# Kernel tuning notes

Hardware: AMD Instinct MI355X
Metric: run time of the kernel (lower is better)

The kernel has to match this reference:

```python
import jax, jax.numpy as jnp
import numpy as np

H, HKV, D = 32, 8, 128          # query heads, kv heads, head dim
G = H // HKV                     # GQA group size
PAGE, TOPK = 64, 64              # page size, top-k pages per (b, kv-head)
SCALE = D ** -0.5


def rotate_half(x):
    x1, x2 = x[..., : x.shape[-1] // 2], x[..., x.shape[-1] // 2 :]
    return jnp.concatenate((-x2, x1), axis=-1)


def setup_inputs() -> dict:
    key = jax.random.key(0)
    ks = jax.random.split(key, 8)
    B, Q, HID, S = 4, 1, 4096, 16384
    hidden_states = jax.random.normal(ks[0], (B, Q, HID), jnp.float32)
    # rotary embedding for current decode position S
    inv_freq = 1.0 / (10000.0 ** (np.arange(0, D, 2, dtype=np.float32) / D))
    ang = np.float32(S) * inv_freq
    emb = np.concatenate([ang, ang])  # [D]
    cos = jnp.broadcast_to(jnp.asarray(np.cos(emb))[None, None, :], (B, Q, D)).astype(jnp.float32)
    sin = jnp.broadcast_to(jnp.asarray(np.sin(emb))[None, None, :], (B, Q, D)).astype(jnp.float32)
    k_cache = jax.random.normal(ks[1], (B, HKV, S, D), jnp.float32)
    v_cache = jax.random.normal(ks[2], (B, HKV, S, D), jnp.float32)
    Wq = jax.random.normal(ks[3], (H * D, HID), jnp.float32) * 0.02
    Wk = jax.random.normal(ks[4], (HKV * D, HID), jnp.float32) * 0.02
    Wv = jax.random.normal(ks[5], (HKV * D, HID), jnp.float32) * 0.02
    Wo = jax.random.normal(ks[6], (HID, H * D), jnp.float32) * 0.02
    return dict(hidden_states=hidden_states, cos=cos, sin=sin,
                k_cache=k_cache, v_cache=v_cache, Wq=Wq, Wk=Wk, Wv=Wv, Wo=Wo)


def reference(hidden_states, cos, sin, k_cache, v_cache, Wq, Wk, Wv, Wo):
    B, Q, HID = hidden_states.shape
    S = k_cache.shape[2]
    P = S // PAGE

    # QKV projections (Linear, no bias) -> [B, heads, Q, D]
    q = (hidden_states @ Wq.T).reshape(B, Q, H, D).transpose(0, 2, 1, 3)
    k_new = (hidden_states @ Wk.T).reshape(B, Q, HKV, D).transpose(0, 2, 1, 3)
    v_new = (hidden_states @ Wv.T).reshape(B, Q, HKV, D).transpose(0, 2, 1, 3)

    # RoPE (unsqueeze_dim=1)
    c, s = cos[:, None, :, :], sin[:, None, :, :]
    q = q * c + rotate_half(q) * s
    k_new = k_new * c + rotate_half(k_new) * s

    # merge grouped query heads to kv heads (reduce='mean', merge_mode='kv')
    q_merged = q.reshape(B, HKV, G, Q, D).mean(axis=2)[:, :, 0, :]  # [B, HKV, D]

    # Quest page summaries: per-page elementwise min/max of keys
    Kp = k_cache.reshape(B, HKV, P, PAGE, D)
    Vp = v_cache.reshape(B, HKV, P, PAGE, D)
    kmin = Kp.min(axis=3)  # [B, HKV, P, D]
    kmax = Kp.max(axis=3)
    qm = q_merged[:, :, None, :]
    page_scores = jnp.maximum(qm * kmin, qm * kmax).sum(axis=-1)  # [B, HKV, P]

    # top-k page selection per (batch, kv head), gather selected pages
    _, idx = jax.lax.top_k(page_scores, TOPK)  # [B, HKV, TOPK]
    gidx = idx[:, :, :, None, None]
    K_sel = jnp.take_along_axis(Kp, gidx, axis=2).reshape(B, HKV, TOPK * PAGE, D)
    V_sel = jnp.take_along_axis(Vp, gidx, axis=2).reshape(B, HKV, TOPK * PAGE, D)

    # append current decode token's kv
    K = jnp.concatenate([K_sel, k_new], axis=2)  # [B, HKV, L, D]
    V = jnp.concatenate([V_sel, v_new], axis=2)

    # GQA attention over gathered sparse KV (no mask in quest decode path)
    qg = q.reshape(B, HKV, G, Q, D)
    logits = jnp.einsum('bhgqd,bhld->bhgql', qg, K) * SCALE
    w = jax.nn.softmax(logits.astype(jnp.float32), axis=-1).astype(q.dtype)
    o = jnp.einsum('bhgql,bhld->bhgqd', w, V)              # [B, HKV, G, Q, D]
    o = o.reshape(B, H, Q, D).transpose(0, 2, 1, 3).reshape(B, Q, H * D)
    return o @ Wo.T  # [B, Q, HID]
```

## Files before the change

kernel.cpp:

```cpp
#include <hip/hip_runtime.h>
#include <hip/hip_bf16.h>
#include <math.h>

constexpr int NB    = 4;
constexpr int NHID  = 4096;
constexpr int NHEAD = 32;
constexpr int NKV   = 8;
constexpr int NGQ   = 4;
constexpr int ND    = 128;
constexpr int NS    = 16384;
constexpr int NPG   = 64;
constexpr int NP    = 256;
constexpr int NTOP  = 64;
constexpr int NSPLIT = 32;
constexpr int PPS   = NTOP / NSPLIT;
constexpr float FSCALE = 0.08838834764831845f;

constexpr int QKV_BLOCKS = 6144 / 4;
constexpr int MM_BLOCKS  = NB * NKV * NP;

__global__ __launch_bounds__(256) void k_qkv_minmax(
    const float* __restrict__ hs, const float* __restrict__ Wq,
    const float* __restrict__ Wk, const float* __restrict__ Wv,
    const float* __restrict__ kc, float* __restrict__ qkv,
    float* __restrict__ kmm) {
  int bid = blockIdx.x;
  int t = threadIdx.x;
  if (bid < QKV_BLOCKS) {
    int row0 = bid * 4;
    const float4* x4 = (const float4*)hs;
    const float4* wr[4];
#pragma unroll
    for (int r = 0; r < 4; r++) {
      int row = row0 + r;
      const float* w;
      if (row < 4096)      w = Wq + (size_t)row * NHID;
      else if (row < 5120) w = Wk + (size_t)(row - 4096) * NHID;
      else                 w = Wv + (size_t)(row - 5120) * NHID;
      wr[r] = (const float4*)w;
    }
    float acc[4][4] = {};
    for (int j = t; j < NHID / 4; j += 256) {
      float4 x0 = x4[j], x1 = x4[1024 + j], x2 = x4[2048 + j], x3 = x4[3072 + j];
#pragma unroll
      for (int r = 0; r < 4; r++) {
        float4 w4 = wr[r][j];
        acc[r][0] += w4.x * x0.x + w4.y * x0.y + w4.z * x0.z + w4.w * x0.w;
        acc[r][1] += w4.x * x1.x + w4.y * x1.y + w4.z * x1.z + w4.w * x1.w;
        acc[r][2] += w4.x * x2.x + w4.y * x2.y + w4.z * x2.z + w4.w * x2.w;
        acc[r][3] += w4.x * x3.x + w4.y * x3.y + w4.z * x3.z + w4.w * x3.w;
      }
    }
    __shared__ float red[4][16];
    int lane = t & 63, wv = t >> 6;
#pragma unroll
    for (int r = 0; r < 4; r++)
#pragma unroll
      for (int b = 0; b < 4; b++) {
        float v = acc[r][b];
        v += __shfl_down(v, 32); v += __shfl_down(v, 16); v += __shfl_down(v, 8);
        v += __shfl_down(v, 4);  v += __shfl_down(v, 2);  v += __shfl_down(v, 1);
        if (lane == 0) red[wv][r * 4 + b] = v;
      }
    __syncthreads();
    if (t < 16) {
      int r = t >> 2, b = t & 3;
      float s = red[0][t] + red[1][t] + red[2][t] + red[3][t];
      qkv[(size_t)b * 6144 + row0 + r] = s;
    }
  } else {
    int pid = bid - QKV_BLOCKS;
    const float4* Kp = (const float4*)(kc + (size_t)pid * NPG * ND);
    int c4 = t & 31, rg = t >> 5;
    float4 mn = make_float4(INFINITY, INFINITY, INFINITY, INFINITY);
    float4 mx = make_float4(-INFINITY, -INFINITY, -INFINITY, -INFINITY);
#pragma unroll
    for (int r = 0; r < 8; r++) {
      float4 v = Kp[(rg * 8 + r) * 32 + c4];
      mn.x = fminf(mn.x, v.x); mn.y = fminf(mn.y, v.y);
      mn.z = fminf(mn.z, v.z); mn.w = fminf(mn.w, v.w);
      mx.x = fmaxf(mx.x, v.x); mx.y = fmaxf(mx.y, v.y);
      mx.z = fmaxf(mx.z, v.z); mx.w = fmaxf(mx.w, v.w);
    }
    __shared__ float4 smn[8][32], smx[8][32];
    smn[rg][c4] = mn; smx[rg][c4] = mx;
    __syncthreads();
    if (t < 32) {
      float4 a = smn[0][t], b4 = smx[0][t];
#pragma unroll
      for (int r = 1; r < 8; r++) {
        float4 u = smn[r][t], w = smx[r][t];
        a.x = fminf(a.x, u.x); a.y = fminf(a.y, u.y);
        a.z = fminf(a.z, u.z); a.w = fminf(a.w, u.w);
        b4.x = fmaxf(b4.x, w.x); b4.y = fmaxf(b4.y, w.y);
        b4.z = fmaxf(b4.z, w.z); b4.w = fmaxf(b4.w, w.w);
      }
      float4* dst = (float4*)kmm + (size_t)pid * 64;
      dst[t] = a;
      dst[32 + t] = b4;
    }
  }
}

__global__ __launch_bounds__(256) void k_rope_score_topk(
    const float* __restrict__ qkv, const float* __restrict__ cosp,
    const float* __restrict__ sinp, const float* __restrict__ kmm,
    float* __restrict__ qr, float* __restrict__ kn, float* __restrict__ vn,
    int* __restrict__ sel) {
  int bh = blockIdx.x;
  int b = bh >> 3, kv = bh & 7;
  const float* cs = cosp + b * ND;
  const float* sn = sinp + b * ND;
  int t = threadIdx.x;
  int g = t >> 6, i = t & 63;
  __shared__ float sq[4][ND];
  __shared__ __align__(16) float qmS[ND];
  __shared__ float sc[NP];
  {
    int h = kv * NGQ + g;
    const float* q = qkv + (size_t)b * 6144 + h * ND;
    float x1 = q[i], x2 = q[i + 64];
    float o1 = x1 * cs[i] - x2 * sn[i];
    float o2 = x2 * cs[i + 64] + x1 * sn[i + 64];
    float* dst = qr + ((size_t)b * NHEAD + h) * ND;
    dst[i] = o1; dst[i + 64] = o2;
    sq[g][i] = o1; sq[g][i + 64] = o2;
  }
  if (t < 64) {
    const float* k = qkv + (size_t)b * 6144 + 4096 + kv * ND;
    float x1 = k[t], x2 = k[t + 64];
    float* dst = kn + (size_t)bh * ND;
    dst[t] = x1 * cs[t] - x2 * sn[t];
    dst[t + 64] = x2 * cs[t + 64] + x1 * sn[t + 64];
  }
  if (t < 128) {
    vn[(size_t)bh * ND + t] = qkv[(size_t)b * 6144 + 5120 + kv * ND + t];
  }
  __syncthreads();
  if (t < 128) {
    qmS[t] = 0.25f * (sq[0][t] + sq[1][t] + sq[2][t] + sq[3][t]);
  }
  __syncthreads();
#pragma unroll
  for (int rd = 0; rd < 4; rd++) {
    int p = (t >> 2) + rd * 64;
    int q = t & 3;
    const float4* mm = (const float4*)kmm + ((size_t)bh * NP + p) * 64;
    float s = 0.f;
#pragma unroll
    for (int j = 0; j < 8; j++) {
      float4 mn = mm[q * 8 + j];
      float4 mx = mm[32 + q * 8 + j];
      const float4 qv = *(const float4*)&qmS[q * 32 + j * 4];
      s += fmaxf(qv.x * mn.x, qv.x * mx.x);
      s += fmaxf(qv.y * mn.y, qv.y * mx.y);
      s += fmaxf(qv.z * mn.z, qv.z * mx.z);
      s += fmaxf(qv.w * mn.w, qv.w * mx.w);
    }
    s += __shfl_xor(s, 1); s += __shfl_xor(s, 2);
    if (q == 0) sc[p] = s;
  }
  __syncthreads();
  float mine = sc[t];
  int rank = 0;
  for (int j = 0; j < NP; j++) {
    float v = sc[j];
    rank += (v > mine) || (v == mine && j < t);
  }
  if (rank < NTOP) sel[(size_t)bh * NTOP + rank] = t;
}

__global__ __launch_bounds__(256) void k_attn_part(
    const float* __restrict__ kc, const float* __restrict__ vc,
    const float* __restrict__ qr, const int* __restrict__ sel,
    float* __restrict__ part_l, float* __restrict__ part_o) {
  int idx = blockIdx.x;
  int sp = idx & (NSPLIT - 1);
  int bh = idx / NSPLIT;
  int b = bh >> 3, kv = bh & 7;
  int t = threadIdx.x;
  int g = t >> 6, lane = t & 63;
  int h = kv * NGQ + g;
  int half = lane >> 5;
  int li = lane & 31;
  const float4* q4 = (const float4*)(qr + ((size_t)b * NHEAD + h) * ND);
  float4 qv = q4[li];
  float lsum = 0.f;
  float4 o = make_float4(0.f, 0.f, 0.f, 0.f);
#pragma unroll
  for (int pi = 0; pi < PPS; pi++) {
    int page = sel[(size_t)bh * NTOP + sp * PPS + pi];
    const float4* Kp = (const float4*)(kc + ((size_t)bh * NS + (size_t)page * NPG) * ND);
    const float4* Vp = (const float4*)(vc + ((size_t)bh * NS + (size_t)page * NPG) * ND);
    for (int r2 = 0; r2 < NPG / 2; r2++) {
      int r = r2 * 2 + half;
      float4 kk = Kp[r * 32 + li];
      float d = kk.x * qv.x + kk.y * qv.y + kk.z * qv.z + kk.w * qv.w;
      d += __shfl_xor(d, 1); d += __shfl_xor(d, 2); d += __shfl_xor(d, 4);
      d += __shfl_xor(d, 8); d += __shfl_xor(d, 16);
      float w = __expf(d * FSCALE);
      lsum += w;
      float4 vv = Vp[r * 32 + li];
      o.x += w * vv.x; o.y += w * vv.y; o.z += w * vv.z; o.w += w * vv.w;
    }
  }
  o.x += __shfl_xor(o.x, 32); o.y += __shfl_xor(o.y, 32);
  o.z += __shfl_xor(o.z, 32); o.w += __shfl_xor(o.w, 32);
  lsum += __shfl_xor(lsum, 32);
  if (half == 0) {
    float4* po = (float4*)(part_o + (((size_t)bh * NGQ + g) * NSPLIT + sp) * ND);
    po[li] = o;
    if (li == 0) part_l[((size_t)bh * NGQ + g) * NSPLIT + sp] = lsum;
  }
}

__global__ __launch_bounds__(64) void k_combine(
    const float* __restrict__ qr, const float* __restrict__ kn,
    const float* __restrict__ vn, const float* __restrict__ part_l,
    const float* __restrict__ part_o, float* __restrict__ attno) {
  int bid = blockIdx.x;
  int b = bid >> 5, h = bid & 31;
  int kv = h >> 2, g = h & 3;
  int lane = threadIdx.x;
  int bh = b * NKV + kv;
  const float2* q2 = (const float2*)(qr + ((size_t)b * NHEAD + h) * ND);
  const float2* k2 = (const float2*)(kn + (size_t)bh * ND);
  float2 qv = q2[lane], kk = k2[lane];
  float d = qv.x * kk.x + qv.y * kk.y;
  d += __shfl_xor(d, 1); d += __shfl_xor(d, 2); d += __shfl_xor(d, 4);
  d += __shfl_xor(d, 8); d += __shfl_xor(d, 16); d += __shfl_xor(d, 32);
  float wn = __expf(d * FSCALE);
  const float2* v2 = (const float2*)(vn + (size_t)bh * ND);
  float2 vv = v2[lane];
  float ox = wn * vv.x, oy = wn * vv.y, lt = wn;
  const float* pl = part_l + ((size_t)bh * NGQ + g) * NSPLIT;
  const float2* po = (const float2*)(part_o + (((size_t)bh * NGQ + g) * NSPLIT) * ND);
  for (int s = 0; s < NSPLIT; s++) {
    lt += pl[s];
    float2 p = po[(size_t)s * 64 + lane];
    ox += p.x; oy += p.y;
  }
  float inv = 1.0f / lt;
  float2* ao = (float2*)(attno + ((size_t)b * NHEAD + h) * ND);
  ao[lane] = make_float2(ox * inv, oy * inv);
}

__global__ __launch_bounds__(256) void k_oproj(
    const float* __restrict__ Wo, const float* __restrict__ x,
    float* __restrict__ out) {
  int row0 = blockIdx.x * 4;
  int t = threadIdx.x;
  const float4* x4 = (const float4*)x;
  float acc[4][4] = {};
  for (int j = t; j < NHID / 4; j += 256) {
    float4 x0 = x4[j], x1 = x4[1024 + j], x2 = x4[2048 + j], x3 = x4[3072 + j];
#pragma unroll
    for (int r = 0; r < 4; r++) {
      float4 w4 = ((const float4*)(Wo + (size_t)(row0 + r) * NHID))[j];
      acc[r][0] += w4.x * x0.x + w4.y * x0.y + w4.z * x0.z + w4.w * x0.w;
      acc[r][1] += w4.x * x1.x + w4.y * x1.y + w4.z * x1.z + w4.w * x1.w;
      acc[r][2] += w4.x * x2.x + w4.y * x2.y + w4.z * x2.z + w4.w * x2.w;
      acc[r][3] += w4.x * x3.x + w4.y * x3.y + w4.z * x3.z + w4.w * x3.w;
    }
  }
  __shared__ float red[4][16];
  int lane = t & 63, wv = t >> 6;
#pragma unroll
  for (int r = 0; r < 4; r++)
#pragma unroll
    for (int b = 0; b < 4; b++) {
      float v = acc[r][b];
      v += __shfl_down(v, 32); v += __shfl_down(v, 16); v += __shfl_down(v, 8);
      v += __shfl_down(v, 4);  v += __shfl_down(v, 2);  v += __shfl_down(v, 1);
      if (lane == 0) red[wv][r * 4 + b] = v;
    }
  __syncthreads();
  if (t < 16) {
    int r = t >> 2, b = t & 3;
    float s = red[0][t] + red[1][t] + red[2][t] + red[3][t];
    out[(size_t)b * NHID + row0 + r] = s;
  }
}

extern "C" void kernel_launch(void* const* d_in, const int* in_sizes, int n_in,
                              void* d_out, int out_size, void* d_ws, size_t ws_size,
                              hipStream_t stream) {
  const float* hs   = (const float*)d_in[0];
  const float* cosp = (const float*)d_in[1];
  const float* sinp = (const float*)d_in[2];
  const float* kc   = (const float*)d_in[3];
  const float* vc   = (const float*)d_in[4];
  const float* Wq   = (const float*)d_in[5];
  const float* Wk   = (const float*)d_in[6];
  const float* Wv   = (const float*)d_in[7];
  const float* Wo   = (const float*)d_in[8];
  float* out = (float*)d_out;

  float* ws = (float*)d_ws;
  float* qkv    = ws;
  float* qr     = ws + 24576;
  float* kn     = ws + 40960;
  float* vn     = ws + 45056;
  float* kmm    = ws + 49152;
  int*   sel    = (int*)(ws + 2146304);
  float* part_l = ws + 2148352;
  float* part_o = ws + 2152448;
  float* attno  = ws + 2676736;

  k_qkv_minmax<<<QKV_BLOCKS + MM_BLOCKS, 256, 0, stream>>>(hs, Wq, Wk, Wv, kc, qkv, kmm);
  k_rope_score_topk<<<NB * NKV, 256, 0, stream>>>(qkv, cosp, sinp, kmm, qr, kn, vn, sel);
  k_attn_part<<<NB * NKV * NSPLIT, 256, 0, stream>>>(kc, vc, qr, sel, part_l, part_o);
  k_combine<<<NB * NHEAD, 64, 0, stream>>>(qr, kn, vn, part_l, part_o, attno);
  k_oproj<<<NHID / 4, 256, 0, stream>>>(Wo, attno, out);
}
```

Baseline: 130.7 us.

## Fuse split-attention combine into partial kernel via last-block atomic counter

Merges the separate combine kernel into the partial-attention kernel. Each split block bumps a per-(batch, kv-head) atomic counter after writing its partials, and the last block to arrive does the reduction. The counter is reset in the top-k kernel. The two-page inner loop is also interleaved so both pages' loads and shuffles are issued together for more memory-level parallelism. This removes one kernel launch, at the cost of a threadfence, an atomic per block and a serialized tail reduction done by one block.

New measurement: 235.3 us. 1.8x slower.

```diff
diff --git a/kernel.cpp b/kernel.cpp
--- a/kernel.cpp
+++ b/kernel.cpp
@@ -13,7 +13,6 @@
 constexpr int NP    = 256;
 constexpr int NTOP  = 64;
 constexpr int NSPLIT = 32;
-constexpr int PPS   = NTOP / NSPLIT;
 constexpr float FSCALE = 0.08838834764831845f;
 
 constexpr int QKV_BLOCKS = 6144 / 4;
@@ -106,7 +105,7 @@
     const float* __restrict__ qkv, const float* __restrict__ cosp,
     const float* __restrict__ sinp, const float* __restrict__ kmm,
     float* __restrict__ qr, float* __restrict__ kn, float* __restrict__ vn,
-    int* __restrict__ sel) {
+    int* __restrict__ sel, int* __restrict__ cnt) {
   int bh = blockIdx.x;
   int b = bh >> 3, kv = bh & 7;
   const float* cs = cosp + b * ND;
@@ -116,6 +115,7 @@
   __shared__ float sq[4][ND];
   __shared__ __align__(16) float qmS[ND];
   __shared__ float sc[NP];
+  if (t == 0) cnt[bh] = 0;
   {
     int h = kv * NGQ + g;
     const float* q = qkv + (size_t)b * 6144 + h * ND;
@@ -170,10 +170,11 @@
   if (rank < NTOP) sel[(size_t)bh * NTOP + rank] = t;
 }
 
-__global__ __launch_bounds__(256) void k_attn_part(
+__global__ __launch_bounds__(256) void k_attn_combine(
     const float* __restrict__ kc, const float* __restrict__ vc,
-    const float* __restrict__ qr, const int* __restrict__ sel,
-    float* __restrict__ part_l, float* __restrict__ part_o) {
+    const float* __restrict__ qr, const float* __restrict__ kn,
+    const float* __restrict__ vn, const int* __restrict__ sel,
+    int* cnt, float* part_l, float* part_o, float* __restrict__ attno) {
   int idx = blockIdx.x;
   int sp = idx & (NSPLIT - 1);
   int bh = idx / NSPLIT;
@@ -187,22 +188,32 @@
   float4 qv = q4[li];
   float lsum = 0.f;
   float4 o = make_float4(0.f, 0.f, 0.f, 0.f);
-#pragma unroll
-  for (int pi = 0; pi < PPS; pi++) {
-    int page = sel[(size_t)bh * NTOP + sp * PPS + pi];
-    const float4* Kp = (const float4*)(kc + ((size_t)bh * NS + (size_t)page * NPG) * ND);
-    const float4* Vp = (const float4*)(vc + ((size_t)bh * NS + (size_t)page * NPG) * ND);
-    for (int r2 = 0; r2 < NPG / 2; r2++) {
-      int r = r2 * 2 + half;
-      float4 kk = Kp[r * 32 + li];
-      float d = kk.x * qv.x + kk.y * qv.y + kk.z * qv.z + kk.w * qv.w;
-      d += __shfl_xor(d, 1); d += __shfl_xor(d, 2); d += __shfl_xor(d, 4);
-      d += __shfl_xor(d, 8); d += __shfl_xor(d, 16);
-      float w = __expf(d * FSCALE);
-      lsum += w;
-      float4 vv = Vp[r * 32 + li];
-      o.x += w * vv.x; o.y += w * vv.y; o.z += w * vv.z; o.w += w * vv.w;
-    }
+  int page0 = sel[(size_t)bh * NTOP + sp * 2];
+  int page1 = sel[(size_t)bh * NTOP + sp * 2 + 1];
+  const float4* K0 = (const float4*)(kc + ((size_t)bh * NS + (size_t)page0 * NPG) * ND);
+  const float4* V0 = (const float4*)(vc + ((size_t)bh * NS + (size_t)page0 * NPG) * ND);
+  const float4* K1 = (const float4*)(kc + ((size_t)bh * NS + (size_t)page1 * NPG) * ND);
+  const float4* V1 = (const float4*)(vc + ((size_t)bh * NS + (size_t)page1 * NPG) * ND);
+  for (int r2 = 0; r2 < NPG / 2; r2++) {
+    int r = r2 * 2 + half;
+    float4 ka = K0[r * 32 + li];
+    float4 kb = K1[r * 32 + li];
+    float d0 = ka.x * qv.x + ka.y * qv.y + ka.z * qv.z + ka.w * qv.w;
+    float d1 = kb.x * qv.x + kb.y * qv.y + kb.z * qv.z + kb.w * qv.w;
+    d0 += __shfl_xor(d0, 1); d1 += __shfl_xor(d1, 1);
+    d0 += __shfl_xor(d0, 2); d1 += __shfl_xor(d1, 2);
+    d0 += __shfl_xor(d0, 4); d1 += __shfl_xor(d1, 4);
+    d0 += __shfl_xor(d0, 8); d1 += __shfl_xor(d1, 8);
+    d0 += __shfl_xor(d0, 16); d1 += __shfl_xor(d1, 16);
+    float w0 = __expf(d0 * FSCALE);
+    float w1 = __expf(d1 * FSCALE);
+    lsum += w0 + w1;
+    float4 va = V0[r * 32 + li];
+    float4 vb = V1[r * 32 + li];
+    o.x += w0 * va.x + w1 * vb.x;
+    o.y += w0 * va.y + w1 * vb.y;
+    o.z += w0 * va.z + w1 * vb.z;
+    o.w += w0 * va.w + w1 * vb.w;
   }
   o.x += __shfl_xor(o.x, 32); o.y += __shfl_xor(o.y, 32);
   o.z += __shfl_xor(o.z, 32); o.w += __shfl_xor(o.w, 32);
@@ -212,33 +223,38 @@
     po[li] = o;
     if (li == 0) part_l[((size_t)bh * NGQ + g) * NSPLIT + sp] = lsum;
   }
-}
-
-__global__ __launch_bounds__(64) void k_combine(
-    const float* __restrict__ qr, const float* __restrict__ kn,
-    const float* __restrict__ vn, const float* __restrict__ part_l,
-    const float* __restrict__ part_o, float* __restrict__ attno) {
-  int bid = blockIdx.x;
-  int b = bid >> 5, h = bid & 31;
-  int kv = h >> 2, g = h & 3;
-  int lane = threadIdx.x;
-  int bh = b * NKV + kv;
+  __threadfence();
+  __shared__ int isLast;
+  if (t == 0) {
+    int old = __hip_atomic_fetch_add(&cnt[bh], 1, __ATOMIC_ACQ_REL,
+                                     __HIP_MEMORY_SCOPE_AGENT);
+    isLast = (old == NSPLIT - 1);
+  }
+  __syncthreads();
+  if (!isLast) return;
   const float2* q2 = (const float2*)(qr + ((size_t)b * NHEAD + h) * ND);
   const float2* k2 = (const float2*)(kn + (size_t)bh * ND);
-  float2 qv = q2[lane], kk = k2[lane];
-  float d = qv.x * kk.x + qv.y * kk.y;
+  float2 qv2 = q2[lane], kk2 = k2[lane];
+  float d = qv2.x * kk2.x + qv2.y * kk2.y;
   d += __shfl_xor(d, 1); d += __shfl_xor(d, 2); d += __shfl_xor(d, 4);
   d += __shfl_xor(d, 8); d += __shfl_xor(d, 16); d += __shfl_xor(d, 32);
   float wn = __expf(d * FSCALE);
   const float2* v2 = (const float2*)(vn + (size_t)bh * ND);
-  float2 vv = v2[lane];
-  float ox = wn * vv.x, oy = wn * vv.y, lt = wn;
-  const float* pl = part_l + ((size_t)bh * NGQ + g) * NSPLIT;
-  const float2* po = (const float2*)(part_o + (((size_t)bh * NGQ + g) * NSPLIT) * ND);
+  float2 vv2 = v2[lane];
+  float ox = wn * vv2.x, oy = wn * vv2.y;
+  float lp = 0.f;
+  if (lane < 32)
+    lp = __hip_atomic_load(&part_l[((size_t)bh * NGQ + g) * NSPLIT + lane],
+                           __ATOMIC_RELAXED, __HIP_MEMORY_SCOPE_AGENT);
+  lp += __shfl_xor(lp, 1); lp += __shfl_xor(lp, 2); lp += __shfl_xor(lp, 4);
+  lp += __shfl_xor(lp, 8); lp += __shfl_xor(lp, 16); lp += __shfl_xor(lp, 32);
+  float lt = wn + lp;
+  float* pobase = part_o + ((size_t)bh * NGQ + g) * NSPLIT * ND;
   for (int s = 0; s < NSPLIT; s++) {
-    lt += pl[s];
-    float2 p = po[(size_t)s * 64 + lane];
-    ox += p.x; oy += p.y;
+    ox += __hip_atomic_load(pobase + (size_t)s * ND + 2 * lane,
+                            __ATOMIC_RELAXED, __HIP_MEMORY_SCOPE_AGENT);
+    oy += __hip_atomic_load(pobase + (size_t)s * ND + 2 * lane + 1,
+                            __ATOMIC_RELAXED, __HIP_MEMORY_SCOPE_AGENT);
   }
   float inv = 1.0f / lt;
   float2* ao = (float2*)(attno + ((size_t)b * NHEAD + h) * ND);
@@ -303,13 +319,13 @@
   float* vn     = ws + 45056;
   float* kmm    = ws + 49152;
   int*   sel    = (int*)(ws + 2146304);
-  float* part_l = ws + 2148352;
-  float* part_o = ws + 2152448;
-  float* attno  = ws + 2676736;
+  int*   cnt    = (int*)(ws + 2148352);
+  float* part_l = ws + 2148416;
+  float* part_o = ws + 2152512;
+  float* attno  = ws + 2676800;
 
   k_qkv_minmax<<<QKV_BLOCKS + MM_BLOCKS, 256, 0, stream>>>(hs, Wq, Wk, Wv, kc, qkv, kmm);
-  k_rope_score_topk<<<NB * NKV, 256, 0, stream>>>(qkv, cosp, sinp, kmm, qr, kn, vn, sel);
-  k_attn_part<<<NB * NKV * NSPLIT, 256, 0, stream>>>(kc, vc, qr, sel, part_l, part_o);
-  k_combine<<<NB * NHEAD, 64, 0, stream>>>(qr, kn, vn, part_l, part_o, attno);
+  k_rope_score_topk<<<NB * NKV, 256, 0, stream>>>(qkv, cosp, sinp, kmm, qr, kn, vn, sel, cnt);
+  k_attn_combine<<<NB * NKV * NSPLIT, 256, 0, stream>>>(kc, vc, qr, kn, vn, sel, cnt, part_l, part_o, attno);
   k_oproj<<<NHID / 4, 256, 0, stream>>>(Wo, attno, out);
 }
```

## Split QKV/minmax kernel and give each attention block one page with unrolled loads

Applied to the files above, without the earlier changes.

The fused QKV-projection plus page min/max kernel becomes two separate launches. The attention split count doubles so each block handles exactly one selected page. The inner loop is unrolled four rows at a time with interleaved shuffles, and launch bounds request 8 blocks per CU, to raise memory-level parallelism on the gathered K/V reads. The workspace offsets for the larger partial buffers are adjusted to match. The split loses the overlap between the weight-bound projection and the cache-bound min/max scan and adds a launch, while the combine step now has twice as many partials to merge.

Measured after the change: 275.2 us. +110.6%, slower.

```diff
diff --git a/kernel.cpp b/kernel.cpp
--- a/kernel.cpp
+++ b/kernel.cpp
@@ -12,93 +12,89 @@
 constexpr int NPG   = 64;
 constexpr int NP    = 256;
 constexpr int NTOP  = 64;
-constexpr int NSPLIT = 32;
-constexpr int PPS   = NTOP / NSPLIT;
+constexpr int NSPLIT = 64;
 constexpr float FSCALE = 0.08838834764831845f;
 
-constexpr int QKV_BLOCKS = 6144 / 4;
-constexpr int MM_BLOCKS  = NB * NKV * NP;
-
-__global__ __launch_bounds__(256) void k_qkv_minmax(
+__global__ __launch_bounds__(256) void k_qkv(
     const float* __restrict__ hs, const float* __restrict__ Wq,
     const float* __restrict__ Wk, const float* __restrict__ Wv,
-    const float* __restrict__ kc, float* __restrict__ qkv,
-    float* __restrict__ kmm) {
-  int bid = blockIdx.x;
-  int t = threadIdx.x;
-  if (bid < QKV_BLOCKS) {
-    int row0 = bid * 4;
-    const float4* x4 = (const float4*)hs;
-    const float4* wr[4];
+    float* __restrict__ qkv) {
+  int row0 = blockIdx.x * 4;
+  int t = threadIdx.x;
+  const float4* x4 = (const float4*)hs;
+  const float4* wr[4];
+#pragma unroll
+  for (int r = 0; r < 4; r++) {
+    int row = row0 + r;
+    const float* w;
+    if (row < 4096)      w = Wq + (size_t)row * NHID;
+    else if (row < 5120) w = Wk + (size_t)(row - 4096) * NHID;
+    else                 w = Wv + (size_t)(row - 5120) * NHID;
+    wr[r] = (const float4*)w;
+  }
+  float acc[4][4] = {};
+  for (int j = t; j < NHID / 4; j += 256) {
+    float4 x0 = x4[j], x1 = x4[1024 + j], x2 = x4[2048 + j], x3 = x4[3072 + j];
 #pragma unroll
     for (int r = 0; r < 4; r++) {
-      int row = row0 + r;
-      const float* w;
-      if (row < 4096)      w = Wq + (size_t)row * NHID;
-      else if (row < 5120) w = Wk + (size_t)(row - 4096) * NHID;
-      else                 w = Wv + (size_t)(row - 5120) * NHID;
-      wr[r] = (const float4*)w;
-    }
-    float acc[4][4] = {};
-    for (int j = t; j < NHID / 4; j += 256) {
-      float4 x0 = x4[j], x1 = x4[1024 + j], x2 = x4[2048 + j], x3 = x4[3072 + j];
-#pragma unroll
-      for (int r = 0; r < 4; r++) {
-        float4 w4 = wr[r][j];
-        acc[r][0] += w4.x * x0.x + w4.y * x0.y + w4.z * x0.z + w4.w * x0.w;
-        acc[r][1] += w4.x * x1.x + w4.y * x1.y + w4.z * x1.z + w4.w * x1.w;
-        acc[r][2] += w4.x * x2.x + w4.y * x2.y + w4.z * x2.z + w4.w * x2.w;
-        acc[r][3] += w4.x * x3.x + w4.y * x3.y + w4.z * x3.z + w4.w * x3.w;
-      }
-    }
-    __shared__ float red[4][16];
-    int lane = t & 63, wv = t >> 6;
-#pragma unroll
-    for (int r = 0; r < 4; r++)
-#pragma unroll
-      for (int b = 0; b < 4; b++) {
-        float v = acc[r][b];
-        v += __shfl_down(v, 32); v += __shfl_down(v, 16); v += __shfl_down(v, 8);
-        v += __shfl_down(v, 4);  v += __shfl_down(v, 2);  v += __shfl_down(v, 1);
-        if (lane == 0) red[wv][r * 4 + b] = v;
-      }
-    __syncthreads();
-    if (t < 16) {
-      int r = t >> 2, b = t & 3;
-      float s = red[0][t] + red[1][t] + red[2][t] + red[3][t];
-      qkv[(size_t)b * 6144 + row0 + r] = s;
-    }
-  } else {
-    int pid = bid - QKV_BLOCKS;
-    const float4* Kp = (const float4*)(kc + (size_t)pid * NPG * ND);
-    int c4 = t & 31, rg = t >> 5;
-    float4 mn = make_float4(INFINITY, INFINITY, INFINITY, INFINITY);
-    float4 mx = make_float4(-INFINITY, -INFINITY, -INFINITY, -INFINITY);
-#pragma unroll
-    for (int r = 0; r < 8; r++) {
-      float4 v = Kp[(rg * 8 + r) * 32 + c4];
-      mn.x = fminf(mn.x, v.x); mn.y = fminf(mn.y, v.y);
-      mn.z = fminf(mn.z, v.z); mn.w = fminf(mn.w, v.w);
-      mx.x = fmaxf(mx.x, v.x); mx.y = fmaxf(mx.y, v.y);
-      mx.z = fmaxf(mx.z, v.z); mx.w = fmaxf(mx.w, v.w);
-    }
-    __shared__ float4 smn[8][32], smx[8][32];
-    smn[rg][c4] = mn; smx[rg][c4] = mx;
-    __syncthreads();
-    if (t < 32) {
-      float4 a = smn[0][t], b4 = smx[0][t];
-#pragma unroll
-      for (int r = 1; r < 8; r++) {
-        float4 u = smn[r][t], w = smx[r][t];
-        a.x = fminf(a.x, u.x); a.y = fminf(a.y, u.y);
-        a.z = fminf(a.z, u.z); a.w = fminf(a.w, u.w);
-        b4.x = fmaxf(b4.x, w.x); b4.y = fmaxf(b4.y, w.y);
-        b4.z = fmaxf(b4.z, w.z); b4.w = fmaxf(b4.w, w.w);
-      }
-      float4* dst = (float4*)kmm + (size_t)pid * 64;
-      dst[t] = a;
-      dst[32 + t] = b4;
-    }
+      float4 w4 = wr[r][j];
+      acc[r][0] += w4.x * x0.x + w4.y * x0.y + w4.z * x0.z + w4.w * x0.w;
+      acc[r][1] += w4.x * x1.x + w4.y * x1.y + w4.z * x1.z + w4.w * x1.w;
+      acc[r][2] += w4.x * x2.x + w4.y * x2.y + w4.z * x2.z + w4.w * x2.w;
+      acc[r][3] += w4.x * x3.x + w4.y * x3.y + w4.z * x3.z + w4.w * x3.w;
+    }
+  }
+  __shared__ float red[4][16];
+  int lane = t & 63, wv = t >> 6;
+#pragma unroll
+  for (int r = 0; r < 4; r++)
+#pragma unroll
+    for (int b = 0; b < 4; b++) {
+      float v = acc[r][b];
+      v += __shfl_down(v, 32); v += __shfl_down(v, 16); v += __shfl_down(v, 8);
+      v += __shfl_down(v, 4);  v += __shfl_down(v, 2);  v += __shfl_down(v, 1);
+      if (lane == 0) red[wv][r * 4 + b] = v;
+    }
+  __syncthreads();
+  if (t < 16) {
+    int r = t >> 2, b = t & 3;
+    float s = red[0][t] + red[1][t] + red[2][t] + red[3][t];
+    qkv[(size_t)b * 6144 + row0 + r] = s;
+  }
+}
+
+__global__ __launch_bounds__(256) void k_minmax(
+    const float* __restrict__ kc, float* __restrict__ kmm) {
+  int pid = blockIdx.x;
+  int t = threadIdx.x;
+  const float4* Kp = (const float4*)(kc + (size_t)pid * NPG * ND);
+  int c4 = t & 31, rg = t >> 5;
+  float4 mn = make_float4(INFINITY, INFINITY, INFINITY, INFINITY);
+  float4 mx = make_float4(-INFINITY, -INFINITY, -INFINITY, -INFINITY);
+#pragma unroll
+  for (int r = 0; r < 8; r++) {
+    float4 v = Kp[(rg * 8 + r) * 32 + c4];
+    mn.x = fminf(mn.x, v.x); mn.y = fminf(mn.y, v.y);
+    mn.z = fminf(mn.z, v.z); mn.w = fminf(mn.w, v.w);
+    mx.x = fmaxf(mx.x, v.x); mx.y = fmaxf(mx.y, v.y);
+    mx.z = fmaxf(mx.z, v.z); mx.w = fmaxf(mx.w, v.w);
+  }
+  __shared__ float4 smn[8][32], smx[8][32];
+  smn[rg][c4] = mn; smx[rg][c4] = mx;
+  __syncthreads();
+  if (t < 32) {
+    float4 a = smn[0][t], b4 = smx[0][t];
+#pragma unroll
+    for (int r = 1; r < 8; r++) {
+      float4 u = smn[r][t], w = smx[r][t];
+      a.x = fminf(a.x, u.x); a.y = fminf(a.y, u.y);
+      a.z = fminf(a.z, u.z); a.w = fminf(a.w, u.w);
+      b4.x = fmaxf(b4.x, w.x); b4.y = fmaxf(b4.y, w.y);
+      b4.z = fmaxf(b4.z, w.z); b4.w = fmaxf(b4.w, w.w);
+    }
+    float4* dst = (float4*)kmm + (size_t)pid * 64;
+    dst[t] = a;
+    dst[32 + t] = b4;
   }
 }
 
@@ -170,7 +166,7 @@
   if (rank < NTOP) sel[(size_t)bh * NTOP + rank] = t;
 }
 
-__global__ __launch_bounds__(256) void k_attn_part(
+__global__ __launch_bounds__(256, 8) void k_attn_part(
     const float* __restrict__ kc, const float* __restrict__ vc,
     const float* __restrict__ qr, const int* __restrict__ sel,
     float* __restrict__ part_l, float* __restrict__ part_o) {
@@ -187,22 +183,43 @@
   float4 qv = q4[li];
   float lsum = 0.f;
   float4 o = make_float4(0.f, 0.f, 0.f, 0.f);
-#pragma unroll
-  for (int pi = 0; pi < PPS; pi++) {
-    int page = sel[(size_t)bh * NTOP + sp * PPS + pi];
-    const float4* Kp = (const float4*)(kc + ((size_t)bh * NS + (size_t)page * NPG) * ND);
-    const float4* Vp = (const float4*)(vc + ((size_t)bh * NS + (size_t)page * NPG) * ND);
-    for (int r2 = 0; r2 < NPG / 2; r2++) {
-      int r = r2 * 2 + half;
-      float4 kk = Kp[r * 32 + li];
-      float d = kk.x * qv.x + kk.y * qv.y + kk.z * qv.z + kk.w * qv.w;
-      d += __shfl_xor(d, 1); d += __shfl_xor(d, 2); d += __shfl_xor(d, 4);
-      d += __shfl_xor(d, 8); d += __shfl_xor(d, 16);
-      float w = __expf(d * FSCALE);
-      lsum += w;
-      float4 vv = Vp[r * 32 + li];
-      o.x += w * vv.x; o.y += w * vv.y; o.z += w * vv.z; o.w += w * vv.w;
-    }
+  int page = sel[(size_t)bh * NTOP + sp];
+  const float4* Kp = (const float4*)(kc + ((size_t)bh * NS + (size_t)page * NPG) * ND);
+  const float4* Vp = (const float4*)(vc + ((size_t)bh * NS + (size_t)page * NPG) * ND);
+#pragma unroll
+  for (int it = 0; it < 8; it++) {
+    int r0 = it * 8 + half;
+    float4 k0 = Kp[(r0 + 0) * 32 + li];
+    float4 k1 = Kp[(r0 + 2) * 32 + li];
+    float4 k2 = Kp[(r0 + 4) * 32 + li];
+    float4 k3 = Kp[(r0 + 6) * 32 + li];
+    float d0 = k0.x * qv.x + k0.y * qv.y + k0.z * qv.z + k0.w * qv.w;
+    float d1 = k1.x * qv.x + k1.y * qv.y + k1.z * qv.z + k1.w * qv.w;
+    float d2 = k2.x * qv.x + k2.y * qv.y + k2.z * qv.z + k2.w * qv.w;
+    float d3 = k3.x * qv.x + k3.y * qv.y + k3.z * qv.z + k3.w * qv.w;
+    d0 += __shfl_xor(d0, 1);  d1 += __shfl_xor(d1, 1);
+    d2 += __shfl_xor(d2, 1);  d3 += __shfl_xor(d3, 1);
+    d0 += __shfl_xor(d0, 2);  d1 += __shfl_xor(d1, 2);
+    d2 += __shfl_xor(d2, 2);  d3 += __shfl_xor(d3, 2);
+    d0 += __shfl_xor(d0, 4);  d1 += __shfl_xor(d1, 4);
+    d2 += __shfl_xor(d2, 4);  d3 += __shfl_xor(d3, 4);
+    d0 += __shfl_xor(d0, 8);  d1 += __shfl_xor(d1, 8);
+    d2 += __shfl_xor(d2, 8);  d3 += __shfl_xor(d3, 8);
+    d0 += __shfl_xor(d0, 16); d1 += __shfl_xor(d1, 16);
+    d2 += __shfl_xor(d2, 16); d3 += __shfl_xor(d3, 16);
+    float w0 = __expf(d0 * FSCALE);
+    float w1 = __expf(d1 * FSCALE);
+    float w2 = __expf(d2 * FSCALE);
+    float w3 = __expf(d3 * FSCALE);
+    lsum += (w0 + w1) + (w2 + w3);
+    float4 v0 = Vp[(r0 + 0) * 32 + li];
+    float4 v1 = Vp[(r0 + 2) * 32 + li];
+    float4 v2 = Vp[(r0 + 4) * 32 + li];
+    float4 v3 = Vp[(r0 + 6) * 32 + li];
+    o.x += w0 * v0.x + w1 * v1.x + w2 * v2.x + w3 * v3.x;
+    o.y += w0 * v0.y + w1 * v1.y + w2 * v2.y + w3 * v3.y;
+    o.z += w0 * v0.z + w1 * v1.z + w2 * v2.z + w3 * v3.z;
+    o.w += w0 * v0.w + w1 * v1.w + w2 * v2.w + w3 * v3.w;
   }
   o.x += __shfl_xor(o.x, 32); o.y += __shfl_xor(o.y, 32);
   o.z += __shfl_xor(o.z, 32); o.w += __shfl_xor(o.w, 32);
@@ -304,10 +321,11 @@
   float* kmm    = ws + 49152;
   int*   sel    = (int*)(ws + 2146304);
   float* part_l = ws + 2148352;
-  float* part_o = ws + 2152448;
-  float* attno  = ws + 2676736;
-
-  k_qkv_minmax<<<QKV_BLOCKS + MM_BLOCKS, 256, 0, stream>>>(hs, Wq, Wk, Wv, kc, qkv, kmm);
+  float* part_o = ws + 2156544;
+  float* attno  = ws + 3205120;
+
+  k_qkv<<<6144 / 4, 256, 0, stream>>>(hs, Wq, Wk, Wv, qkv);
+  k_minmax<<<NB * NKV * NP, 256, 0, stream>>>(kc, kmm);
   k_rope_score_topk<<<NB * NKV, 256, 0, stream>>>(qkv, cosp, sinp, kmm, qr, kn, vn, sel);
   k_attn_part<<<NB * NKV * NSPLIT, 256, 0, stream>>>(kc, vc, qr, sel, part_l, part_o);
   k_combine<<<NB * NHEAD, 64, 0, stream>>>(qr, kn, vn, part_l, part_o, attno);
```
